# Kernel optimization log

Measured on AMD Instinct MI355X. Metric: run time of the kernel, lower is better.

## Reference

```python
import jax, jax.numpy as jnp
import numpy as np

B, S, DIM = 4, 2048, 768
H, HD, QK, R = 12, 64, 32, 8  # nheads, head_dim, qk_dim, nrules
EPS = 1e-5


def _ln(x, g, b):
    m = jnp.mean(x, axis=-1, keepdims=True)
    v = jnp.mean((x - m) ** 2, axis=-1, keepdims=True)
    return (x - m) / jnp.sqrt(v + EPS) * g + b


def setup_inputs() -> dict:
    key = jax.random.key(0)
    ks = jax.random.split(key, 12)
    w = lambda k, sh: (jax.random.normal(k, sh, jnp.float32) * 0.02)
    return {
        "x": jax.random.normal(ks[0], (B, S, DIM), jnp.float32),
        "Wq": w(ks[1], (DIM, DIM)), "bq": jnp.zeros((DIM,), jnp.float32),
        "Wk": w(ks[2], (DIM, DIM)), "bk": jnp.zeros((DIM,), jnp.float32),
        "Wv": w(ks[3], (DIM, HD * R)), "bv": jnp.zeros((HD * R,), jnp.float32),
        "Wqv": w(ks[4], (DIM, QK * H)), "bqv": jnp.zeros((QK * H,), jnp.float32),
        "Ws": w(ks[5], (QK + HD, 1)), "bs": jnp.zeros((1,), jnp.float32),
        "Wf": w(ks[6], (DIM, DIM)), "bf": jnp.zeros((DIM,), jnp.float32),
        "W1": w(ks[7], (DIM, 2 * DIM)), "b1": jnp.zeros((2 * DIM,), jnp.float32),
        "W2": w(ks[8], (2 * DIM, DIM)), "b2": jnp.zeros((DIM,), jnp.float32),
        "g1": jnp.ones((DIM,), jnp.float32), "be1": jnp.zeros((DIM,), jnp.float32),
        "g2": jnp.ones((DIM,), jnp.float32), "be2": jnp.zeros((DIM,), jnp.float32),
    }


def reference(x, Wq, bq, Wk, bk, Wv, bv, Wqv, bqv, Ws, bs, Wf, bf,
              W1, b1, W2, b2, g1, be1, g2, be2):
    b, n, _ = x.shape
    res = x
    xn = _ln(x, g1, be1)  # norm_before=True

    # --- stage 1: standard per-head attention, shared across rules ---
    q = (xn @ Wq + bq).reshape(b, n, H, HD) / np.sqrt(HD)
    k = (xn @ Wk + bk).reshape(b, n, H, HD)
    v = (xn @ Wv + bv).reshape(b, n, R, HD)
    score = jax.nn.softmax(jnp.einsum("bqhd,bkhd->bhqk", q, k), axis=-1)
    out = jnp.einsum("bhqk,bkrd->bqhrd", score, v)  # [B,S,H,R,hd]

    # --- stage 2: rule composition via score_network (dot=False) ---
    qv = (xn @ Wqv + bqv).reshape(b, n, H, QK) / np.sqrt(QK)
    # score_network(cat(q_v, out)) == q_v @ Ws[:QK] + out @ Ws[QK:] + bs
    ws_q, ws_o = Ws[:QK, 0], Ws[QK:, 0]
    comp = (jnp.einsum("bqhrd,d->bqhr", out, ws_o)
            + jnp.einsum("bqhk,k->bqh", qv, ws_q)[..., None] + bs[0])
    prev = comp[..., None]  # [B,S,H,R,1] raw scores, returned as `prev`

    rule_w = jax.nn.softmax(comp, axis=-1)  # softmax over rules
    o = jnp.einsum("bqhr,bqhrd->bqhd", rule_w, out).reshape(b, n, DIM)
    o = o @ Wf + bf

    out1 = res + o
    # post-block MLP (dropout inactive at inference)
    on = _ln(out1, g2, be2)
    mlp = jax.nn.relu(on @ W1 + b1) @ W2 + b2
    return out1 + mlp, prev
```

## Files before the change

### kernel.cpp

```cpp
#include <hip/hip_runtime.h>
#include <hip/hip_bf16.h>

typedef __bf16 bfrag  __attribute__((ext_vector_type(8)));
typedef __bf16 bf16x4 __attribute__((ext_vector_type(4)));
typedef float  f32x4  __attribute__((ext_vector_type(4)));

#define MFMA(a,b,c) __builtin_amdgcn_mfma_f32_16x16x32_bf16(a,b,c,0,0,0)

__device__ __forceinline__ void gl_lds16(const void* g, void* l) {
  __builtin_amdgcn_global_load_lds((const __attribute__((address_space(1))) void*)g,
                                   (__attribute__((address_space(3))) void*)l, 16, 0, 0);
}
__device__ __forceinline__ float fexp2(float x) {
  float r;
  asm("v_exp_f32 %0, %1" : "=v"(r) : "v"(x));
  return r;
}
__device__ __forceinline__ unsigned cvtpk(float lo, float hi) {
  unsigned r;
  asm("v_cvt_pk_bf16_f32 %0, %1, %2" : "=v"(r) : "v"(lo), "v"(hi));
  return r;
}

#define NC 2432

#define OFF_C     ((size_t)0)
#define OFF_VT    ((size_t)52428800)
#define OFF_QDOT  ((size_t)61079552)
#define OFF_WCAT  ((size_t)61472768)
#define OFF_BCAT  ((size_t)65208320)
#define OFF_WFT   ((size_t)65218048)
#define OFF_W1T   ((size_t)66397696)
#define OFF_W2T   ((size_t)68756992)
#define OFF_ATTNO ((size_t)71116288)
#define OFF_XN    ((size_t)39845888)
#define OFF_OUT1  ((size_t)0)
#define OFF_ON    ((size_t)12582912)
#define OFF_H1    ((size_t)25165824)

template<typename TIN>
__global__ __launch_bounds__(256) void k_ln(const TIN* __restrict__ in,
    const float* __restrict__ g, const float* __restrict__ be, __bf16* __restrict__ out) {
  int row  = blockIdx.x * 4 + (threadIdx.x >> 6);
  int lane = threadIdx.x & 63;
  const TIN* rp = in + (size_t)row * 768;
  float v[12];
  #pragma unroll
  for (int i = 0; i < 3; i++) {
    int c = i * 256 + lane * 4;
    if constexpr (sizeof(TIN) == 4) {
      float4 lv = *(const float4*)(rp + c);
      v[i*4+0] = lv.x; v[i*4+1] = lv.y; v[i*4+2] = lv.z; v[i*4+3] = lv.w;
    } else {
      bf16x4 lv = *(const bf16x4*)(rp + c);
      #pragma unroll
      for (int jj = 0; jj < 4; jj++) v[i*4+jj] = (float)lv[jj];
    }
  }
  float s = 0.f, sq = 0.f;
  #pragma unroll
  for (int k = 0; k < 12; k++) { s += v[k]; sq += v[k]*v[k]; }
  #pragma unroll
  for (int d = 1; d < 64; d <<= 1) { s += __shfl_xor(s, d); sq += __shfl_xor(sq, d); }
  float mean = s * (1.f/768.f);
  float rstd = rsqrtf(sq * (1.f/768.f) - mean*mean + 1e-5f);
  #pragma unroll
  for (int i = 0; i < 3; i++) {
    int c = i * 256 + lane * 4;
    float4 gv = *(const float4*)(g + c);
    float4 bv = *(const float4*)(be + c);
    bf16x4 o;
    o[0] = (__bf16)((v[i*4+0]-mean)*rstd*gv.x + bv.x);
    o[1] = (__bf16)((v[i*4+1]-mean)*rstd*gv.y + bv.y);
    o[2] = (__bf16)((v[i*4+2]-mean)*rstd*gv.z + bv.z);
    o[3] = (__bf16)((v[i*4+3]-mean)*rstd*gv.w + bv.w);
    *(bf16x4*)(out + (size_t)row*768 + c) = o;
  }
}

__global__ __launch_bounds__(256) void k_packT(const float* __restrict__ src, __bf16* __restrict__ dst,
                                               int N, int K, int total) {
  int idx = blockIdx.x * 256 + threadIdx.x;
  if (idx >= total) return;
  int K8 = K >> 3;
  int n = idx / K8, k0 = (idx % K8) * 8;
  bfrag o;
  #pragma unroll
  for (int i = 0; i < 8; i++) o[i] = (__bf16)src[(size_t)(k0+i)*N + n];
  *(bfrag*)&dst[(size_t)n*K + k0] = o;
}

__global__ __launch_bounds__(256) void k_packcat(
    const float* __restrict__ Wq, const float* __restrict__ Wk,
    const float* __restrict__ Wv, const float* __restrict__ Wqv,
    const float* __restrict__ bq, const float* __restrict__ bk,
    const float* __restrict__ bv, const float* __restrict__ bqv,
    __bf16* __restrict__ Wt, float* __restrict__ bcat) {
  int idx = blockIdx.x * 256 + threadIdx.x;
  if (idx >= 2432 * 96) return;
  int n = idx / 96, k0 = (idx % 96) * 8;
  const float* src; int col, sN; float sc = 1.f;
  if (n < 768)       { src = Wq;  col = n;        sN = 768; sc = 0.125f; }
  else if (n < 1536) { src = Wk;  col = n - 768;  sN = 768; }
  else if (n < 2048) { src = Wv;  col = n - 1536; sN = 512; }
  else               { src = Wqv; col = n - 2048; sN = 384; sc = 0.1767766952966369f; }
  bfrag o;
  #pragma unroll
  for (int i = 0; i < 8; i++) o[i] = (__bf16)(src[(size_t)(k0+i)*sN + col] * sc);
  *(bfrag*)&Wt[(size_t)n*768 + k0] = o;
  if (k0 == 0) {
    float bb;
    if (n < 768) bb = bq[col]*0.125f;
    else if (n < 1536) bb = bk[col];
    else if (n < 2048) bb = bv[col];
    else bb = bqv[col]*0.1767766952966369f;
    bcat[n] = bb;
  }
}

template<int KD, int EPI>
__global__ __launch_bounds__(256, 3) void k_gemm(const __bf16* __restrict__ A,
    const __bf16* __restrict__ Bt, const float* __restrict__ bias,
    const float* __restrict__ resf, const __bf16* __restrict__ resb,
    void* __restrict__ Cout, int N) {
  __shared__ __bf16 Al[2][128*32];
  __shared__ __bf16 Bl[2][128*32];
  const int m0 = blockIdx.x * 128, n0 = blockIdx.y * 128;
  const int tid = threadIdx.x, lane = tid & 63, w = tid >> 6;
  const int wm = (w >> 1) * 64, wn = (w & 1) * 64;
  const int srow = lane >> 2, skoff = (lane & 3) * 8;
  const int l15 = lane & 15, lg = lane >> 4;
  f32x4 acc[4][4];
  #pragma unroll
  for (int i = 0; i < 4; i++)
    #pragma unroll
    for (int j = 0; j < 4; j++) acc[i][j] = (f32x4){0.f,0.f,0.f,0.f};
  const int NT = KD / 32;
  auto stage = [&](int buf, int k0) {
    #pragma unroll
    for (int i = 0; i < 2; i++) {
      int c = w * 2 + i;
      gl_lds16(A  + (size_t)(m0 + c*16 + srow) * KD + k0 + skoff, &Al[buf][c*512]);
      gl_lds16(Bt + (size_t)(n0 + c*16 + srow) * KD + k0 + skoff, &Bl[buf][c*512]);
    }
  };
  stage(0, 0);
  __syncthreads();
  for (int t = 0; t < NT; t++) {
    int buf = t & 1;
    if (t + 1 < NT) stage(buf ^ 1, (t + 1) * 32);
    bfrag af[4], bfm[4];
    #pragma unroll
    for (int f = 0; f < 4; f++) {
      af[f]  = *(const bfrag*)&Al[buf][(wm + f*16 + l15)*32 + lg*8];
      bfm[f] = *(const bfrag*)&Bl[buf][(wn + f*16 + l15)*32 + lg*8];
    }
    #pragma unroll
    for (int i = 0; i < 4; i++)
      #pragma unroll
      for (int j = 0; j < 4; j++)
        acc[i][j] = MFMA(af[i], bfm[j], acc[i][j]);
    __syncthreads();
  }
  #pragma unroll
  for (int i = 0; i < 4; i++) {
    int row0 = m0 + wm + i*16 + lg*4;
    #pragma unroll
    for (int j = 0; j < 4; j++) {
      int col = n0 + wn + j*16 + l15;
      float bv = bias[col];
      #pragma unroll
      for (int q = 0; q < 4; q++) {
        size_t r = (size_t)(row0 + q);
        float v = acc[i][j][q] + bv;
        if (EPI == 0)      ((__bf16*)Cout)[r*N + col] = (__bf16)v;
        else if (EPI == 1) { v += resf[r*N + col]; ((__bf16*)Cout)[r*N + col] = (__bf16)v; }
        else if (EPI == 2) ((__bf16*)Cout)[r*N + col] = (__bf16)fmaxf(v, 0.f);
        else               { v += (float)resb[r*N + col]; ((float*)Cout)[r*N + col] = v; }
      }
    }
  }
}

__global__ __launch_bounds__(256) void k_vt(const __bf16* __restrict__ C, const float* __restrict__ Ws,
                                            __bf16* __restrict__ VT) {
  int bid = blockIdx.x;
  int b = bid >> 8, dt = (bid >> 5) & 7, kt = bid & 31;
  __shared__ __bf16 tile[64][72];
  int tid = threadIdx.x;
  int r = tid >> 3, c0 = (tid & 7) * 8;
  #pragma unroll
  for (int p = 0; p < 2; p++) {
    int rr = r + p * 32;
    bfrag v = *(const bfrag*)&C[(size_t)(b*2048 + kt*64 + rr)*NC + 1536 + dt*64 + c0];
    *(bfrag*)&tile[rr][c0] = v;
  }
  __syncthreads();
  #pragma unroll
  for (int p = 0; p < 2; p++) {
    int d = r + p * 32;
    bfrag o;
    #pragma unroll
    for (int i = 0; i < 8; i++) o[i] = tile[c0 + i][d];
    *(bfrag*)&VT[((size_t)b*528 + dt*64 + d)*2048 + kt*64 + c0] = o;
  }
  if (tid < 64) {
    float s = 0.f;
    #pragma unroll
    for (int d = 0; d < 64; d++) s += (float)tile[tid][d] * Ws[32 + d];
    VT[((size_t)b*528 + 512 + dt)*2048 + kt*64 + tid] = (__bf16)s;
  }
}

__global__ __launch_bounds__(256) void k_qdot(const __bf16* __restrict__ C, const float* __restrict__ Ws,
                                              const float* __restrict__ bs, float* __restrict__ qd) {
  int idx = blockIdx.x * 256 + threadIdx.x;
  if (idx >= 98304) return;
  int h = idx % 12; size_t srow = (size_t)(idx / 12);
  const __bf16* qp = &C[srow*NC + 2048 + h*32];
  float s = bs[0];
  #pragma unroll
  for (int j = 0; j < 32; j++) s += (float)qp[j] * Ws[j];
  qd[idx] = s;
}

__global__ __launch_bounds__(512, 2) void k_attn(const __bf16* __restrict__ C,
    const __bf16* __restrict__ VT,
    const float* __restrict__ qdot, __bf16* __restrict__ attno, float* __restrict__ prevout) {
  __shared__ __align__(16) char smem[53248];
  __bf16* Pl   = (__bf16*)(smem);
  __bf16* kbuf = (__bf16*)(smem + 32768);
  float*  wlb  = (float*)(smem + 49152);
  __bf16* rbuf = (__bf16*)(smem);

  const int tid = threadIdx.x, lane = tid & 63, wid = tid >> 6;
  const int l15 = lane & 15, lg = lane >> 4;
  const int bid = (blockIdx.x & 7) * 96 + (blockIdx.x >> 3);
  const int b = bid / 192, rem = bid % 192, h = rem / 16, qb = rem % 16;
  const int q0 = qb * 128;

  const __bf16* VTb = VT + (size_t)b * 528 * 2048;
  const int kkey = tid >> 3, kch = tid & 7;
  const __bf16* Ksrc0 = C + (size_t)(b*2048 + kkey)*NC + 768 + h*64 + ((kch ^ (kkey & 7)) * 8);

  auto stageK = [&](int t) {
    gl_lds16(Ksrc0 + (size_t)t * 64 * NC, kbuf + (t & 1)*4096 + (size_t)wid*512);
  };
  stageK(0);

  const __bf16* Qbase = C + (size_t)(b*2048 + q0 + wid*16 + l15)*NC + h*64 + lg*8;
  bfrag qf0 = *(const bfrag*)(Qbase);
  bfrag qf1 = *(const bfrag*)(Qbase + 32);

  f32x4 accv[8][4];
  #pragma unroll
  for (int i = 0; i < 8; i++)
    #pragma unroll
    for (int j = 0; j < 4; j++) accv[i][j] = (f32x4){0.f,0.f,0.f,0.f};
  f32x4 compa = (f32x4){0.f,0.f,0.f,0.f};
  float lsc = 0.f;

  auto qk_phase = [&](int tn) {
    const __bf16* kb_ = kbuf + (tn & 1) * 4096;
    f32x4 s[4];
    #pragma unroll
    for (int cf = 0; cf < 4; cf++) s[cf] = (f32x4){0.f,0.f,0.f,0.f};
    #pragma unroll
    for (int cf = 0; cf < 4; cf++) {
      int key = cf*16 + l15, swz = key & 7;
      bfrag ka  = *(const bfrag*)(kb_ + key*64 + ((lg     ^ swz) * 8));
      bfrag kb2 = *(const bfrag*)(kb_ + key*64 + (((lg+4) ^ swz) * 8));
      s[cf] = MFMA(ka, qf0, s[cf]);
      s[cf] = MFMA(kb2, qf1, s[cf]);
    }
    int row = wid*16 + l15;
    char* base = (char*)Pl + (tn & 1)*16384 + row*128;
    int swz = (row & 7) << 4;
    #pragma unroll
    for (int cf = 0; cf < 4; cf++) {
      float p0 = fexp2(s[cf][0] * 1.44269504f);
      float p1 = fexp2(s[cf][1] * 1.44269504f);
      float p2 = fexp2(s[cf][2] * 1.44269504f);
      float p3 = fexp2(s[cf][3] * 1.44269504f);
      lsc += (p0 + p1) + (p2 + p3);
      uint2 pk;
      pk.x = cvtpk(p0, p1);
      pk.y = cvtpk(p2, p3);
      *(uint2*)(base + ((cf*32 + lg*8) ^ swz)) = pk;
    }
  };

  __syncthreads();

  qk_phase(0);
  stageK(1);

  for (int t = 0; t < 32; t++) {
    const int k0 = t * 64, pb = t & 1;
    __syncthreads();
    if (t + 2 < 32) stageK(t + 2);
    const __bf16* vwp = VTb + (size_t)(512 + l15)*2048 + k0 + lg*8;
    bfrag vw0 = *(const bfrag*)(vwp);
    bfrag vw1 = *(const bfrag*)(vwp + 32);
    bfrag vb[4][2];
    #pragma unroll
    for (int cf = 0; cf < 4; cf++) {
      const __bf16* vp = VTb + (size_t)(wid*64 + cf*16 + l15)*2048 + k0 + lg*8;
      vb[cf][0] = *(const bfrag*)(vp);
      vb[cf][1] = *(const bfrag*)(vp + 32);
    }
    if (t < 31) qk_phase(t + 1);
    {
      int prow = wid*16 + l15;
      int swz = (prow & 7) << 4;
      const char* pbase = (const char*)Pl + pb*16384 + prow*128;
      bfrag pa0 = *(const bfrag*)(pbase + ((lg*16) ^ swz));
      bfrag pa1 = *(const bfrag*)(pbase + ((64 + lg*16) ^ swz));
      compa = MFMA(pa0, vw0, compa);
      compa = MFMA(pa1, vw1, compa);
    }
    __builtin_amdgcn_s_setprio(1);
    #pragma unroll
    for (int rf = 0; rf < 8; rf++) {
      int prow = rf*16 + l15;
      int swz = (prow & 7) << 4;
      const char* pbase = (const char*)Pl + pb*16384 + prow*128;
      bfrag pa0 = *(const bfrag*)(pbase + ((lg*16) ^ swz));
      bfrag pa1 = *(const bfrag*)(pbase + ((64 + lg*16) ^ swz));
      #pragma unroll
      for (int cf = 0; cf < 4; cf++) {
        accv[rf][cf] = MFMA(pa0, vb[cf][0], accv[rf][cf]);
        accv[rf][cf] = MFMA(pa1, vb[cf][1], accv[rf][cf]);
      }
    }
    __builtin_amdgcn_s_setprio(0);
  }
  float lfall = lsc;
  lfall += __shfl_xor(lfall, 16);
  lfall += __shfl_xor(lfall, 32);
  float lf[4];
  #pragma unroll
  for (int j = 0; j < 4; j++) lf[j] = __shfl(lfall, lg*4 + j);
  {
    int rowg = b*2048 + q0 + wid*16 + lg*4;
    float cmp[4];
    #pragma unroll
    for (int j = 0; j < 4; j++) {
      float qdv = qdot[(size_t)(rowg + j)*12 + h];
      cmp[j] = (l15 < 8) ? (compa[j] / lf[j] + qdv) : -INFINITY;
      if (l15 < 8) prevout[((size_t)(rowg + j)*12 + h)*8 + l15] = cmp[j];
    }
    #pragma unroll
    for (int j = 0; j < 4; j++) {
      float rm = cmp[j];
      rm = fmaxf(rm, __shfl_xor(rm, 1));
      rm = fmaxf(rm, __shfl_xor(rm, 2));
      rm = fmaxf(rm, __shfl_xor(rm, 4));
      float e = exp2f((cmp[j] - rm) * 1.44269504f);
      float rs = e;
      rs += __shfl_xor(rs, 1); rs += __shfl_xor(rs, 2); rs += __shfl_xor(rs, 4);
      float wp = e / (rs * lf[j]);
      if (l15 < 8) wlb[(wid*16 + lg*4 + j)*8 + l15] = wp;
    }
  }
  __syncthreads();
  #pragma unroll
  for (int c = 0; c < 4; c++) {
    #pragma unroll
    for (int rr = 0; rr < 2; rr++) {
      int rf = c*2 + rr;
      #pragma unroll
      for (int j = 0; j < 4; j++) {
        int row = rf*16 + lg*4 + j;
        int lrow = row - c*32;
        float wp = wlb[row*8 + wid];
        #pragma unroll
        for (int cf = 0; cf < 4; cf++)
          rbuf[((size_t)wid*32 + lrow)*64 + cf*16 + l15] = (__bf16)(accv[rf][cf][j] * wp);
      }
    }
    __syncthreads();
    {
      int row32 = tid >> 4, dc = (tid & 15) * 4;
      float os[4] = {0,0,0,0};
      #pragma unroll
      for (int r = 0; r < 8; r++) {
        bf16x4 v = *(const bf16x4*)&rbuf[((size_t)r*32 + row32)*64 + dc];
        #pragma unroll
        for (int i = 0; i < 4; i++) os[i] += (float)v[i];
      }
      int grow = c*32 + row32;
      bf16x4 ov;
      #pragma unroll
      for (int i = 0; i < 4; i++) ov[i] = (__bf16)os[i];
      *(bf16x4*)&attno[(size_t)(b*2048 + q0 + grow)*768 + h*64 + dc] = ov;
    }
    if (c < 3) __syncthreads();
  }
}

extern "C" void kernel_launch(void* const* d_in, const int* in_sizes, int n_in,
                              void* d_out, int out_size, void* d_ws, size_t ws_size,
                              hipStream_t stream) {
  (void)in_sizes; (void)n_in; (void)out_size; (void)ws_size;
  const float* x   = (const float*)d_in[0];
  const float* Wq  = (const float*)d_in[1];
  const float* bq  = (const float*)d_in[2];
  const float* Wk  = (const float*)d_in[3];
  const float* bk  = (const float*)d_in[4];
  const float* Wv  = (const float*)d_in[5];
  const float* bv  = (const float*)d_in[6];
  const float* Wqv = (const float*)d_in[7];
  const float* bqv = (const float*)d_in[8];
  const float* Ws  = (const float*)d_in[9];
  const float* bs  = (const float*)d_in[10];
  const float* Wf  = (const float*)d_in[11];
  const float* bfp = (const float*)d_in[12];
  const float* W1  = (const float*)d_in[13];
  const float* b1  = (const float*)d_in[14];
  const float* W2  = (const float*)d_in[15];
  const float* b2  = (const float*)d_in[16];
  const float* g1  = (const float*)d_in[17];
  const float* be1 = (const float*)d_in[18];
  const float* g2  = (const float*)d_in[19];
  const float* be2 = (const float*)d_in[20];

  char* ws = (char*)d_ws;
  __bf16* Cbuf  = (__bf16*)(ws + OFF_C);
  __bf16* xn    = (__bf16*)(ws + OFF_XN);
  __bf16* VTb   = (__bf16*)(ws + OFF_VT);
  float*  qdotb = (float*)(ws + OFF_QDOT);
  __bf16* Wcat  = (__bf16*)(ws + OFF_WCAT);
  float*  bcat  = (float*)(ws + OFF_BCAT);
  __bf16* WfT   = (__bf16*)(ws + OFF_WFT);
  __bf16* W1T   = (__bf16*)(ws + OFF_W1T);
  __bf16* W2T   = (__bf16*)(ws + OFF_W2T);
  __bf16* attno = (__bf16*)(ws + OFF_ATTNO);
  __bf16* out1  = (__bf16*)(ws + OFF_OUT1);
  __bf16* onb   = (__bf16*)(ws + OFF_ON);
  __bf16* h1    = (__bf16*)(ws + OFF_H1);
  float*  outp  = (float*)d_out;
  float*  prevp = outp + 6291456;

  k_ln<float><<<2048, 256, 0, stream>>>(x, g1, be1, xn);
  k_packcat<<<(2432*96 + 255)/256, 256, 0, stream>>>(Wq, Wk, Wv, Wqv, bq, bk, bv, bqv, Wcat, bcat);
  k_packT<<<(768*96 + 255)/256, 256, 0, stream>>>(Wf, WfT, 768, 768, 768*96);
  k_packT<<<(1536*96 + 255)/256, 256, 0, stream>>>(W1, W1T, 1536, 768, 1536*96);
  k_packT<<<(768*192 + 255)/256, 256, 0, stream>>>(W2, W2T, 768, 1536, 768*192);

  k_gemm<768, 0><<<dim3(64, 19), 256, 0, stream>>>(xn, Wcat, bcat, nullptr, nullptr, Cbuf, NC);

  k_vt<<<1024, 256, 0, stream>>>(Cbuf, Ws, VTb);
  k_qdot<<<384, 256, 0, stream>>>(Cbuf, Ws, bs, qdotb);

  k_attn<<<768, 512, 0, stream>>>(Cbuf, VTb, qdotb, attno, prevp);

  k_gemm<768, 1><<<dim3(64, 6), 256, 0, stream>>>(attno, WfT, bfp, x, nullptr, out1, 768);
  k_ln<__bf16><<<2048, 256, 0, stream>>>(out1, g2, be2, onb);
  k_gemm<768, 2><<<dim3(64, 12), 256, 0, stream>>>(onb, W1T, b1, nullptr, nullptr, h1, 1536);
  k_gemm<1536, 3><<<dim3(64, 6), 256, 0, stream>>>(h1, W2T, b2, nullptr, out1, outp, 768);
}
```

Measured before the change: 536.5 us.

## Split QK phase to interleave exp/softmax with PV MFMAs; swizzle GEMM block order

The attention loop's QK step is split into an MFMA part and a finish part (exp, pack, LDS store). The finish now runs between two halves of the PV MFMA loop, so its latency can overlap with matrix work. Separately, the GEMM remaps blockIdx.x with an 8x8 swizzle to change the order in which M tiles are scheduled, aiming for better cache locality. The interleave raises register pressure because the score fragments stay live across the PV loop.

```diff
diff --git a/kernel.cpp b/kernel.cpp
--- a/kernel.cpp
+++ b/kernel.cpp
@@ -125,7 +125,8 @@
     void* __restrict__ Cout, int N) {
   __shared__ __bf16 Al[2][128*32];
   __shared__ __bf16 Bl[2][128*32];
-  const int m0 = blockIdx.x * 128, n0 = blockIdx.y * 128;
+  const int bx = (blockIdx.x & 7) * 8 + (blockIdx.x >> 3);
+  const int m0 = bx * 128, n0 = blockIdx.y * 128;
   const int tid = threadIdx.x, lane = tid & 63, w = tid >> 6;
   const int wm = (w >> 1) * 64, wn = (w & 1) * 64;
   const int srow = lane >> 2, skoff = (lane & 3) * 8;
@@ -260,9 +261,8 @@
   f32x4 compa = (f32x4){0.f,0.f,0.f,0.f};
   float lsc = 0.f;
 
-  auto qk_phase = [&](int tn) {
+  auto qk_mfma = [&](int tn, f32x4* s) {
     const __bf16* kb_ = kbuf + (tn & 1) * 4096;
-    f32x4 s[4];
     #pragma unroll
     for (int cf = 0; cf < 4; cf++) s[cf] = (f32x4){0.f,0.f,0.f,0.f};
     #pragma unroll
@@ -273,6 +273,8 @@
       s[cf] = MFMA(ka, qf0, s[cf]);
       s[cf] = MFMA(kb2, qf1, s[cf]);
     }
+  };
+  auto qk_finish = [&](int tn, f32x4* s) {
     int row = wid*16 + l15;
     char* base = (char*)Pl + (tn & 1)*16384 + row*128;
     int swz = (row & 7) << 4;
@@ -292,7 +294,11 @@
 
   __syncthreads();
 
-  qk_phase(0);
+  {
+    f32x4 s0[4];
+    qk_mfma(0, s0);
+    qk_finish(0, s0);
+  }
   stageK(1);
 
   for (int t = 0; t < 32; t++) {
@@ -309,7 +315,8 @@
       vb[cf][0] = *(const bfrag*)(vp);
       vb[cf][1] = *(const bfrag*)(vp + 32);
     }
-    if (t < 31) qk_phase(t + 1);
+    f32x4 s[4];
+    if (t < 31) qk_mfma(t + 1, s);
     {
       int prow = wid*16 + l15;
       int swz = (prow & 7) << 4;
@@ -321,7 +328,23 @@
     }
     __builtin_amdgcn_s_setprio(1);
     #pragma unroll
-    for (int rf = 0; rf < 8; rf++) {
+    for (int rf = 0; rf < 4; rf++) {
+      int prow = rf*16 + l15;
+      int swz = (prow & 7) << 4;
+      const char* pbase = (const char*)Pl + pb*16384 + prow*128;
+      bfrag pa0 = *(const bfrag*)(pbase + ((lg*16) ^ swz));
+      bfrag pa1 = *(const bfrag*)(pbase + ((64 + lg*16) ^ swz));
+      #pragma unroll
+      for (int cf = 0; cf < 4; cf++) {
+        accv[rf][cf] = MFMA(pa0, vb[cf][0], accv[rf][cf]);
+        accv[rf][cf] = MFMA(pa1, vb[cf][1], accv[rf][cf]);
+      }
+    }
+    __builtin_amdgcn_s_setprio(0);
+    if (t < 31) qk_finish(t + 1, s);
+    __builtin_amdgcn_s_setprio(1);
+    #pragma unroll
+    for (int rf = 4; rf < 8; rf++) {
       int prow = rf*16 + l15;
       int swz = (prow & 7) << 4;
       const char* pbase = (const char*)Pl + pb*16384 + prow*128;
```

Measured after the change: 538.6 us. Within noise of the previous version (+0.4%).

## Compute rule scores from PV accumulators instead of extra MFMA on projected V

Applied to the files above, without the earlier changes.

Instead of precomputing V·ws_o rows in the transpose kernel and running an extra P×vw MFMA per key tile, the attention kernel now derives each rule's composition score after the loop by dotting the accumulated output tiles with ws_o via cross-lane shuffles and an LDS exchange. This removes per-iteration global loads and MFMAs from the hot loop and shrinks the VT buffer. It adds an epilogue reduction and an extra barrier, and changes rounding because the score now comes from fp32 accumulators rather than bf16-projected values. Separately, the GEMM block index is permuted along M to change the block-to-CU/cache mapping.

```diff
diff --git a/kernel.cpp b/kernel.cpp
--- a/kernel.cpp
+++ b/kernel.cpp
@@ -125,7 +125,8 @@
     void* __restrict__ Cout, int N) {
   __shared__ __bf16 Al[2][128*32];
   __shared__ __bf16 Bl[2][128*32];
-  const int m0 = blockIdx.x * 128, n0 = blockIdx.y * 128;
+  const int bx = (blockIdx.x & 7) * 8 + (blockIdx.x >> 3);
+  const int m0 = bx * 128, n0 = blockIdx.y * 128;
   const int tid = threadIdx.x, lane = tid & 63, w = tid >> 6;
   const int wm = (w >> 1) * 64, wn = (w & 1) * 64;
   const int srow = lane >> 2, skoff = (lane & 3) * 8;
@@ -182,8 +183,7 @@
   }
 }
 
-__global__ __launch_bounds__(256) void k_vt(const __bf16* __restrict__ C, const float* __restrict__ Ws,
-                                            __bf16* __restrict__ VT) {
+__global__ __launch_bounds__(256) void k_vt(const __bf16* __restrict__ C, __bf16* __restrict__ VT) {
   int bid = blockIdx.x;
   int b = bid >> 8, dt = (bid >> 5) & 7, kt = bid & 31;
   __shared__ __bf16 tile[64][72];
@@ -202,13 +202,7 @@
     bfrag o;
     #pragma unroll
     for (int i = 0; i < 8; i++) o[i] = tile[c0 + i][d];
-    *(bfrag*)&VT[((size_t)b*528 + dt*64 + d)*2048 + kt*64 + c0] = o;
-  }
-  if (tid < 64) {
-    float s = 0.f;
-    #pragma unroll
-    for (int d = 0; d < 64; d++) s += (float)tile[tid][d] * Ws[32 + d];
-    VT[((size_t)b*528 + 512 + dt)*2048 + kt*64 + tid] = (__bf16)s;
+    *(bfrag*)&VT[((size_t)b*512 + dt*64 + d)*2048 + kt*64 + c0] = o;
   }
 }
 
@@ -225,7 +219,7 @@
 }
 
 __global__ __launch_bounds__(512, 2) void k_attn(const __bf16* __restrict__ C,
-    const __bf16* __restrict__ VT,
+    const __bf16* __restrict__ VT, const float* __restrict__ Ws,
     const float* __restrict__ qdot, __bf16* __restrict__ attno, float* __restrict__ prevout) {
   __shared__ __align__(16) char smem[53248];
   __bf16* Pl   = (__bf16*)(smem);
@@ -239,7 +233,7 @@
   const int b = bid / 192, rem = bid % 192, h = rem / 16, qb = rem % 16;
   const int q0 = qb * 128;
 
-  const __bf16* VTb = VT + (size_t)b * 528 * 2048;
+  const __bf16* VTb = VT + (size_t)b * 512 * 2048;
   const int kkey = tid >> 3, kch = tid & 7;
   const __bf16* Ksrc0 = C + (size_t)(b*2048 + kkey)*NC + 768 + h*64 + ((kch ^ (kkey & 7)) * 8);
 
@@ -257,7 +251,6 @@
   for (int i = 0; i < 8; i++)
     #pragma unroll
     for (int j = 0; j < 4; j++) accv[i][j] = (f32x4){0.f,0.f,0.f,0.f};
-  f32x4 compa = (f32x4){0.f,0.f,0.f,0.f};
   float lsc = 0.f;
 
   auto qk_phase = [&](int tn) {
@@ -299,9 +292,6 @@
     const int k0 = t * 64, pb = t & 1;
     __syncthreads();
     if (t + 2 < 32) stageK(t + 2);
-    const __bf16* vwp = VTb + (size_t)(512 + l15)*2048 + k0 + lg*8;
-    bfrag vw0 = *(const bfrag*)(vwp);
-    bfrag vw1 = *(const bfrag*)(vwp + 32);
     bfrag vb[4][2];
     #pragma unroll
     for (int cf = 0; cf < 4; cf++) {
@@ -310,15 +300,6 @@
       vb[cf][1] = *(const bfrag*)(vp + 32);
     }
     if (t < 31) qk_phase(t + 1);
-    {
-      int prow = wid*16 + l15;
-      int swz = (prow & 7) << 4;
-      const char* pbase = (const char*)Pl + pb*16384 + prow*128;
-      bfrag pa0 = *(const bfrag*)(pbase + ((lg*16) ^ swz));
-      bfrag pa1 = *(const bfrag*)(pbase + ((64 + lg*16) ^ swz));
-      compa = MFMA(pa0, vw0, compa);
-      compa = MFMA(pa1, vw1, compa);
-    }
     __builtin_amdgcn_s_setprio(1);
     #pragma unroll
     for (int rf = 0; rf < 8; rf++) {
@@ -341,13 +322,33 @@
   float lf[4];
   #pragma unroll
   for (int j = 0; j < 4; j++) lf[j] = __shfl(lfall, lg*4 + j);
+
+  {
+    float wso = Ws[32 + l15];
+    float wso1 = Ws[32 + 16 + l15];
+    float wso2 = Ws[32 + 32 + l15];
+    float wso3 = Ws[32 + 48 + l15];
+    #pragma unroll
+    for (int rf = 0; rf < 8; rf++) {
+      #pragma unroll
+      for (int j = 0; j < 4; j++) {
+        float cj = accv[rf][0][j]*wso + accv[rf][1][j]*wso1
+                 + accv[rf][2][j]*wso2 + accv[rf][3][j]*wso3;
+        cj += __shfl_xor(cj, 1); cj += __shfl_xor(cj, 2);
+        cj += __shfl_xor(cj, 4); cj += __shfl_xor(cj, 8);
+        if (l15 == 0) wlb[(rf*16 + lg*4 + j)*8 + wid] = cj;
+      }
+    }
+  }
+  __syncthreads();
   {
     int rowg = b*2048 + q0 + wid*16 + lg*4;
     float cmp[4];
     #pragma unroll
     for (int j = 0; j < 4; j++) {
       float qdv = qdot[(size_t)(rowg + j)*12 + h];
-      cmp[j] = (l15 < 8) ? (compa[j] / lf[j] + qdv) : -INFINITY;
+      float cv = (l15 < 8) ? wlb[(wid*16 + lg*4 + j)*8 + l15] : 0.f;
+      cmp[j] = (l15 < 8) ? (cv / lf[j] + qdv) : -INFINITY;
       if (l15 < 8) prevout[((size_t)(rowg + j)*12 + h)*8 + l15] = cmp[j];
     }
     #pragma unroll
@@ -450,10 +451,10 @@
 
   k_gemm<768, 0><<<dim3(64, 19), 256, 0, stream>>>(xn, Wcat, bcat, nullptr, nullptr, Cbuf, NC);
 
-  k_vt<<<1024, 256, 0, stream>>>(Cbuf, Ws, VTb);
+  k_vt<<<1024, 256, 0, stream>>>(Cbuf, VTb);
   k_qdot<<<384, 256, 0, stream>>>(Cbuf, Ws, bs, qdotb);
 
-  k_attn<<<768, 512, 0, stream>>>(Cbuf, VTb, qdotb, attno, prevp);
+  k_attn<<<768, 512, 0, stream>>>(Cbuf, VTb, Ws, qdotb, attno, prevp);
 
   k_gemm<768, 1><<<dim3(64, 6), 256, 0, stream>>>(attno, WfT, bfp, x, nullptr, out1, 768);
   k_ln<__bf16><<<2048, 256, 0, stream>>>(out1, g2, be2, onb);
```

Result: faster. 501.2 us (-6.6%).
